# Optimization experiments

Hardware: AMD Instinct MI355X
Metric: run time of the kernel (lower is better)

The kernel has to match this reference:

```python
import jax, jax.numpy as jnp
import numpy as np

N_NODES = 50000
N_EDGES = 800000
NUM_RELATIONS = 8   # 2 * n_speakers**2 with n_speakers = 2
NUM_BASES = 30
G_DIM, H1_DIM, H2_DIM = 128, 128, 128


def setup_inputs() -> dict:
    key = jax.random.key(0)
    ks = jax.random.split(key, 10)
    inp = {
        "node_features": jax.random.normal(ks[0], (N_NODES, G_DIM), jnp.float32),
        "edge_index": jax.random.randint(ks[1], (2, N_EDGES), 0, N_NODES, dtype=jnp.int64),
        "edge_type": jax.random.randint(ks[2], (N_EDGES,), 0, NUM_RELATIONS, dtype=jnp.int64),
        "edge_norm": jax.random.uniform(ks[3], (N_EDGES,), jnp.float32),
        # RGCNConv params (basis decomposition)
        "basis": jax.random.normal(ks[4], (NUM_BASES, G_DIM, H1_DIM), jnp.float32) * 0.05,
        "comp": jax.random.normal(ks[5], (NUM_RELATIONS, NUM_BASES), jnp.float32) * 0.1,
        "root": jax.random.normal(ks[6], (G_DIM, H1_DIM), jnp.float32) * 0.05,
        "bias1": jnp.zeros((H1_DIM,), jnp.float32),
        # GraphConv params: lin_rel (with bias) applied to aggregated neighbors, lin_root (no bias)
        "w_rel": jax.random.normal(ks[7], (H1_DIM, H2_DIM), jnp.float32) * 0.05,
        "b_rel": jnp.zeros((H2_DIM,), jnp.float32),
        "w_root": jax.random.normal(ks[8], (H1_DIM, H2_DIM), jnp.float32) * 0.05,
    }
    return inp


def reference(node_features, edge_index, edge_type, edge_norm,
              basis, comp, root, bias1, w_rel, b_rel, w_root):
    src, dst = edge_index[0], edge_index[1]  # source_to_target flow (PyG default)

    # ---- Layer 1: RGCNConv with basis decomposition ----
    # W[r] = sum_b comp[r,b] * basis[b]  -> [R, g, h1]
    W = jnp.einsum('rb,bio->rio', comp, basis)
    # Project every node under every relation once (N*R*h1), then gather per edge.
    # Mathematically identical to per-edge x_j @ W[edge_type] but avoids an [E, g, h1] tensor.
    x_proj = jnp.einsum('ni,rio->nro', node_features, W)  # [N, R, h1]
    msg = x_proj[src, edge_type] * edge_norm[:, None]     # [E, h1]
    agg = jax.ops.segment_sum(msg, dst, num_segments=N_NODES)  # scatter-add to targets
    h = agg + node_features @ root + bias1                # [N, h1]

    # ---- Layer 2: GraphConv (aggr='add', no edge_weight) ----
    agg2 = jax.ops.segment_sum(h[src], dst, num_segments=N_NODES)  # [N, h1]
    out = agg2 @ w_rel + b_rel + h @ w_root               # [N, h2]
    return out
```

## Files before the change

### kernel.cpp

```cpp
#include <hip/hip_runtime.h>
#include <hip/hip_bf16.h>
#include <stdint.h>

#define N_NODES 50000
#define N_EDGES 800000
#define NREL    8
#define NBASES  30
#define DIM     128
#define NSLOT   9
#define NCAT    (NSLOT*DIM)
#define SCAN_NB ((N_NODES + 255) / 256)

typedef __attribute__((ext_vector_type(8))) short short8;
typedef __attribute__((ext_vector_type(4))) float floatx4;
typedef __hip_bfloat16  bf16;
typedef __hip_bfloat162 bf16x2;

__device__ inline ushort f2bu(float f) { bf16 b = __float2bfloat16(f); return *(ushort*)&b; }
__device__ inline float  bu2f(ushort u) { union { unsigned i; float f; } c; c.i = ((unsigned)u) << 16; return c.f; }

__global__ void prep_weights(const float* __restrict__ basis, const float* __restrict__ comp,
                             const float* __restrict__ root, const float* __restrict__ w_rel,
                             const float* __restrict__ w_root,
                             bf16* __restrict__ WcatT, bf16* __restrict__ wrelT, bf16* __restrict__ wrootT) {
    int idx = blockIdx.x * blockDim.x + threadIdx.x;
    const int n_cat = NCAT * DIM;
    const int n_sq  = DIM * DIM;
    if (idx < n_cat) {
        int k = idx & 127, n = idx >> 7;
        int r = n >> 7, o = n & 127;
        float v;
        if (r < NREL) {
            v = 0.f;
            for (int b = 0; b < NBASES; ++b)
                v += comp[r * NBASES + b] * basis[(b * DIM + k) * DIM + o];
        } else {
            v = root[k * DIM + o];
        }
        WcatT[n * DIM + k] = __float2bfloat16(v);
    } else if (idx < n_cat + n_sq) {
        int t = idx - n_cat; int k = t & 127, o = t >> 7;
        wrelT[o * DIM + k] = __float2bfloat16(w_rel[k * DIM + o]);
    } else if (idx < n_cat + 2 * n_sq) {
        int t = idx - n_cat - n_sq; int k = t & 127, o = t >> 7;
        wrootT[o * DIM + k] = __float2bfloat16(w_root[k * DIM + o]);
    }
}

__global__ void conv_x(const float4* __restrict__ x4, ushort4* __restrict__ xb4, int n4) {
    int i = blockIdx.x * blockDim.x + threadIdx.x;
    if (i < n4) {
        float4 f = x4[i];
        ushort4 o;
        o.x = f2bu(f.x); o.y = f2bu(f.y); o.z = f2bu(f.z); o.w = f2bu(f.w);
        xb4[i] = o;
    }
}

__global__ void hist_kernel(const int* __restrict__ ei, int* __restrict__ deg) {
    int e = blockIdx.x * blockDim.x + threadIdx.x;
    if (e < N_EDGES) atomicAdd(&deg[ei[N_EDGES + e]], 1);
}

__global__ void scan_blocks(const int* __restrict__ deg, int* __restrict__ segoff,
                            int* __restrict__ bsum, int n) {
    __shared__ int buf[256];
    int tid = threadIdx.x;
    int i = blockIdx.x * 256 + tid;
    int v = (i < n) ? deg[i] : 0;
    buf[tid] = v;
    __syncthreads();
#pragma unroll
    for (int o = 1; o < 256; o <<= 1) {
        int t = (tid >= o) ? buf[tid - o] : 0;
        __syncthreads();
        buf[tid] += t;
        __syncthreads();
    }
    if (i < n) segoff[i + 1] = buf[tid];
    if (tid == 255) bsum[blockIdx.x] = buf[255];
}

__global__ void scan_sums(int* __restrict__ bsum, int nb) {
    int lane = threadIdx.x;
    int base = 0;
    for (int start = 0; start < nb; start += 64) {
        int i = start + lane;
        int v = (i < nb) ? bsum[i] : 0;
        int incl = v;
#pragma unroll
        for (int o = 1; o < 64; o <<= 1) {
            int t = __shfl_up(incl, o, 64);
            if (lane >= o) incl += t;
        }
        if (i < nb) bsum[i] = base + incl - v;
        base += __shfl(incl, 63, 64);
    }
}

__global__ void scan_add(int* __restrict__ segoff, const int* __restrict__ bsum, int n) {
    int i = blockIdx.x * 256 + threadIdx.x;
    if (i < n) segoff[i + 1] += bsum[blockIdx.x];
    if (i == 0) segoff[0] = 0;
}

__global__ void scatter_kernel(const int* __restrict__ ei, const int* __restrict__ et,
                               const float* __restrict__ en, const int* __restrict__ segoff,
                               int* __restrict__ cur, uint2* __restrict__ rec) {
    int e = blockIdx.x * blockDim.x + threadIdx.x;
    if (e < N_EDGES) {
        int d = ei[N_EDGES + e];
        int p = segoff[d] + atomicAdd(&cur[d], 1);
        rec[p] = make_uint2((unsigned)ei[e] | ((unsigned)et[e] << 16), __float_as_uint(en[e]));
    }
}

__global__ __launch_bounds__(256) void gemm1_kernel(const bf16* __restrict__ A, const bf16* __restrict__ BT,
                                                    bf16* __restrict__ C, int M) {
    __shared__ ushort As[64][136];
    __shared__ ushort Bs[64][136];
    const ushort* Au = (const ushort*)A;
    const ushort* Bu = (const ushort*)BT;
    ushort* Cu = (ushort*)C;
    int tm = blockIdx.x * 64;
    int wave = threadIdx.x >> 6, lane = threadIdx.x & 63;
    int q = lane >> 4, mr = lane & 15;

#pragma unroll
    for (int u = 0; u < 4; ++u) {
        int cc = threadIdx.x + u * 256;
        int row = cc >> 4, seg = cc & 15;
        int gr = tm + row;
        short8 av = {0, 0, 0, 0, 0, 0, 0, 0};
        if (gr < M) av = *(const short8*)(Au + (size_t)gr * 128 + seg * 8);
        *(short8*)(&As[row][seg * 8]) = av;
    }

    floatx4 zero = {0.f, 0.f, 0.f, 0.f};
    for (int t = 0; t < 18; ++t) {
        if (t) __syncthreads();
#pragma unroll
        for (int u = 0; u < 4; ++u) {
            int cc = threadIdx.x + u * 256;
            int row = cc >> 4, seg = cc & 15;
            short8 bv = *(const short8*)(Bu + (size_t)(t * 64 + row) * 128 + seg * 8);
            *(short8*)(&Bs[row][seg * 8]) = bv;
        }
        __syncthreads();
        floatx4 acc[4] = {zero, zero, zero, zero};
#pragma unroll
        for (int kt = 0; kt < 4; ++kt) {
            short8 a = *(const short8*)(&As[wave * 16 + mr][q * 8 + kt * 32]);
#pragma unroll
            for (int nt = 0; nt < 4; ++nt) {
                short8 b = *(const short8*)(&Bs[nt * 16 + mr][q * 8 + kt * 32]);
                acc[nt] = __builtin_amdgcn_mfma_f32_16x16x32_bf16(a, b, acc[nt], 0, 0, 0);
            }
        }
#pragma unroll
        for (int nt = 0; nt < 4; ++nt)
#pragma unroll
            for (int r4 = 0; r4 < 4; ++r4) {
                int row = tm + wave * 16 + q * 4 + r4;
                if (row < M) Cu[(size_t)row * NCAT + t * 64 + nt * 16 + mr] = f2bu(acc[nt][r4]);
            }
    }
}

__global__ void seg1_kernel(const uint2* __restrict__ rec, const int* __restrict__ segoff,
                            const ushort* __restrict__ proj, const float* __restrict__ bias1,
                            ushort* __restrict__ h) {
    int quad = threadIdx.x >> 4;
    int node = blockIdx.x * 16 + quad;
    if (node >= N_NODES) return;
    int lane = threadIdx.x & 15;
    int s = segoff[node], e = segoff[node + 1];
    float acc[8] = {0.f, 0.f, 0.f, 0.f, 0.f, 0.f, 0.f, 0.f};
    for (int chunk = s; chunk < e; chunk += 4) {
        int m = e - chunk; if (m > 4) m = 4;
        uint2 rr[4]; short8 vv[4];
#pragma unroll
        for (int j = 0; j < 4; ++j) if (j < m) rr[j] = rec[chunk + j];
#pragma unroll
        for (int j = 0; j < 4; ++j) if (j < m) {
            unsigned src = rr[j].x & 0xFFFFu;
            unsigned typ = rr[j].x >> 16;
            vv[j] = *(const short8*)(proj + ((size_t)src * NSLOT + typ) * 128 + lane * 8);
        }
#pragma unroll
        for (int j = 0; j < 4; ++j) if (j < m) {
            float norm = __uint_as_float(rr[j].y);
#pragma unroll
            for (int f = 0; f < 8; ++f) acc[f] += norm * bu2f((ushort)vv[j][f]);
        }
    }
    short8 base = *(const short8*)(proj + ((size_t)node * NSLOT + 8) * 128 + lane * 8);
    short8 o;
#pragma unroll
    for (int f = 0; f < 8; ++f)
        o[f] = (short)f2bu(acc[f] + bu2f((ushort)base[f]) + bias1[lane * 8 + f]);
    *(short8*)(h + (size_t)node * 128 + lane * 8) = o;
}

__global__ void seg2_kernel(const uint2* __restrict__ rec, const int* __restrict__ segoff,
                            const ushort* __restrict__ h, ushort* __restrict__ out2) {
    int quad = threadIdx.x >> 4;
    int node = blockIdx.x * 16 + quad;
    if (node >= N_NODES) return;
    int lane = threadIdx.x & 15;
    int s = segoff[node], e = segoff[node + 1];
    float acc[8] = {0.f, 0.f, 0.f, 0.f, 0.f, 0.f, 0.f, 0.f};
    for (int chunk = s; chunk < e; chunk += 4) {
        int m = e - chunk; if (m > 4) m = 4;
        uint2 rr[4]; short8 vv[4];
#pragma unroll
        for (int j = 0; j < 4; ++j) if (j < m) rr[j] = rec[chunk + j];
#pragma unroll
        for (int j = 0; j < 4; ++j) if (j < m)
            vv[j] = *(const short8*)(h + (size_t)(rr[j].x & 0xFFFFu) * 128 + lane * 8);
#pragma unroll
        for (int j = 0; j < 4; ++j) if (j < m)
#pragma unroll
            for (int f = 0; f < 8; ++f) acc[f] += bu2f((ushort)vv[j][f]);
    }
    short8 o;
#pragma unroll
    for (int f = 0; f < 8; ++f) o[f] = (short)f2bu(acc[f]);
    *(short8*)(out2 + (size_t)node * 128 + lane * 8) = o;
}

__global__ __launch_bounds__(256) void gemm2_kernel(const bf16* __restrict__ A1, const bf16* __restrict__ B1T,
                                                    const bf16* __restrict__ A2, const bf16* __restrict__ B2T,
                                                    const float* __restrict__ brel, float* __restrict__ out, int M) {
    __shared__ ushort As[64][136];
    __shared__ ushort Bs[64][136];
    int tm = blockIdx.x * 64, tn = blockIdx.y * 64;
    int wave = threadIdx.x >> 6, lane = threadIdx.x & 63;
    int q = lane >> 4, mr = lane & 15;
    floatx4 zero = {0.f, 0.f, 0.f, 0.f};
    floatx4 acc[4] = {zero, zero, zero, zero};

    for (int phase = 0; phase < 2; ++phase) {
        const ushort* Au = (const ushort*)(phase ? A2 : A1);
        const ushort* Bu = (const ushort*)(phase ? B2T : B1T);
        if (phase) __syncthreads();
        for (int c = threadIdx.x; c < 64 * 16; c += 256) {
            int row = c >> 4, seg = c & 15;
            int gr = tm + row;
            short8 av = {0, 0, 0, 0, 0, 0, 0, 0};
            if (gr < M) av = *(const short8*)(Au + (size_t)gr * 128 + seg * 8);
            *(short8*)(&As[row][seg * 8]) = av;
            short8 bv = *(const short8*)(Bu + (size_t)(tn + row) * 128 + seg * 8);
            *(short8*)(&Bs[row][seg * 8]) = bv;
        }
        __syncthreads();
#pragma unroll
        for (int kt = 0; kt < 4; ++kt) {
            short8 a = *(const short8*)(&As[wave * 16 + mr][q * 8 + kt * 32]);
#pragma unroll
            for (int nt = 0; nt < 4; ++nt) {
                short8 b = *(const short8*)(&Bs[nt * 16 + mr][q * 8 + kt * 32]);
                acc[nt] = __builtin_amdgcn_mfma_f32_16x16x32_bf16(a, b, acc[nt], 0, 0, 0);
            }
        }
    }
    __syncthreads();
    float* Csf = (float*)&As[0][0];
#pragma unroll
    for (int nt = 0; nt < 4; ++nt)
#pragma unroll
        for (int r4 = 0; r4 < 4; ++r4) {
            int row = wave * 16 + q * 4 + r4;
            int col = nt * 16 + mr;
            Csf[row * 68 + col] = acc[nt][r4] + brel[tn + col];
        }
    __syncthreads();
#pragma unroll
    for (int u = 0; u < 4; ++u) {
        int cc = threadIdx.x + u * 256;
        int row = cc >> 4, seg = cc & 15;
        int gr = tm + row;
        if (gr < M) {
            float4 v = *(const float4*)(&Csf[row * 68 + seg * 4]);
            *(float4*)(out + (size_t)gr * 128 + tn + seg * 4) = v;
        }
    }
}

extern "C" void kernel_launch(void* const* d_in, const int* in_sizes, int n_in,
                              void* d_out, int out_size, void* d_ws, size_t ws_size,
                              hipStream_t stream) {
    const float* x      = (const float*)d_in[0];
    const int*   ei     = (const int*)d_in[1];
    const int*   et     = (const int*)d_in[2];
    const float* en     = (const float*)d_in[3];
    const float* basis  = (const float*)d_in[4];
    const float* comp   = (const float*)d_in[5];
    const float* root   = (const float*)d_in[6];
    const float* bias1  = (const float*)d_in[7];
    const float* w_rel  = (const float*)d_in[8];
    const float* b_rel  = (const float*)d_in[9];
    const float* w_root = (const float*)d_in[10];
    float* out = (float*)d_out;

    char* ws = (char*)d_ws;
    size_t off = 0;
    auto alloc = [&](size_t bytes) { size_t o = off; off += (bytes + 255) & ~(size_t)255; return o; };

    size_t o_deg    = alloc((size_t)N_NODES * 4);
    size_t o_cur    = alloc((size_t)N_NODES * 4);
    size_t o_segoff = alloc((size_t)(N_NODES + 1) * 4);
    size_t o_bsum   = alloc((size_t)SCAN_NB * 4);
    size_t o_rec    = alloc((size_t)N_EDGES * 8);
    size_t o_wcat   = alloc((size_t)NCAT * DIM * 2);
    size_t o_wrel   = alloc((size_t)DIM * DIM * 2);
    size_t o_wroot  = alloc((size_t)DIM * DIM * 2);
    size_t o_xb     = alloc((size_t)N_NODES * DIM * 2);
    size_t o_proj   = alloc((size_t)N_NODES * NCAT * 2);
    size_t o_hb     = alloc((size_t)N_NODES * DIM * 2);
    size_t o_agg2   = alloc((size_t)N_NODES * DIM * 2);

    int*   deg    = (int*)(ws + o_deg);
    int*   cur    = (int*)(ws + o_cur);
    int*   segoff = (int*)(ws + o_segoff);
    int*   bsum   = (int*)(ws + o_bsum);
    uint2* rec    = (uint2*)(ws + o_rec);
    bf16*  wcat   = (bf16*)(ws + o_wcat);
    bf16*  wrelT  = (bf16*)(ws + o_wrel);
    bf16*  wrootT = (bf16*)(ws + o_wroot);
    bf16*  xb     = (bf16*)(ws + o_xb);
    bf16*  proj   = (bf16*)(ws + o_proj);
    bf16*  hb     = (bf16*)(ws + o_hb);
    bf16*  agg2   = (bf16*)(ws + o_agg2);

    hipMemsetAsync(ws + o_deg, 0, o_segoff - o_deg, stream);

    {
        int total = NCAT * DIM + 2 * DIM * DIM;
        prep_weights<<<(total + 255) / 256, 256, 0, stream>>>(basis, comp, root, w_rel, w_root,
                                                              wcat, wrelT, wrootT);
    }
    {
        int n4 = N_NODES * DIM / 4;
        conv_x<<<(n4 + 255) / 256, 256, 0, stream>>>((const float4*)x, (ushort4*)xb, n4);
    }
    hist_kernel<<<(N_EDGES + 255) / 256, 256, 0, stream>>>(ei, deg);
    scan_blocks<<<SCAN_NB, 256, 0, stream>>>(deg, segoff, bsum, N_NODES);
    scan_sums<<<1, 64, 0, stream>>>(bsum, SCAN_NB);
    scan_add<<<SCAN_NB, 256, 0, stream>>>(segoff, bsum, N_NODES);
    scatter_kernel<<<(N_EDGES + 255) / 256, 256, 0, stream>>>(ei, et, en, segoff, cur, rec);

    gemm1_kernel<<<(N_NODES + 63) / 64, 256, 0, stream>>>(xb, wcat, proj, N_NODES);
    seg1_kernel<<<(N_NODES + 15) / 16, 256, 0, stream>>>(rec, segoff, (const ushort*)proj, bias1, (ushort*)hb);
    seg2_kernel<<<(N_NODES + 15) / 16, 256, 0, stream>>>(rec, segoff, (const ushort*)hb, (ushort*)agg2);
    {
        dim3 grid((N_NODES + 63) / 64, DIM / 64);
        gemm2_kernel<<<grid, 256, 0, stream>>>(agg2, wrelT, hb, wrootT, b_rel, out, N_NODES);
    }
}
```

Measured before the change: 336.1 us.

## Replace global atomic edge scatter with two-pass bucketed counting sort

The per-edge scatter that used one global atomic per edge on a per-node counter becomes a two-pass placement. The first pass buckets edges into coarse chunks of 256 destination nodes using shared-memory histograms and one global atomic per block and bucket. The second pass sorts each bucket into per-node segments using shared-memory atomics. This is meant to cut global atomic contention and scattered writes, at the cost of an extra 6.4MB temp buffer, an extra kernel launch, and packing the local destination into the record's high bits.

After: 328.6 us. 1.02x faster.

```diff
diff --git a/kernel.cpp b/kernel.cpp
--- a/kernel.cpp
+++ b/kernel.cpp
@@ -10,6 +10,9 @@
 #define NSLOT   9
 #define NCAT    (NSLOT*DIM)
 #define SCAN_NB ((N_NODES + 255) / 256)
+#define NB_C    196
+#define EPB_PLACE 2048
+#define NBLK_PLACE ((N_EDGES + EPB_PLACE - 1) / EPB_PLACE)
 
 typedef __attribute__((ext_vector_type(8))) short short8;
 typedef __attribute__((ext_vector_type(4))) float floatx4;
@@ -104,14 +107,54 @@
     if (i == 0) segoff[0] = 0;
 }
 
-__global__ void scatter_kernel(const int* __restrict__ ei, const int* __restrict__ et,
-                               const float* __restrict__ en, const int* __restrict__ segoff,
-                               int* __restrict__ cur, uint2* __restrict__ rec) {
-    int e = blockIdx.x * blockDim.x + threadIdx.x;
-    if (e < N_EDGES) {
-        int d = ei[N_EDGES + e];
-        int p = segoff[d] + atomicAdd(&cur[d], 1);
-        rec[p] = make_uint2((unsigned)ei[e] | ((unsigned)et[e] << 16), __float_as_uint(en[e]));
+__global__ __launch_bounds__(256) void place_kernel(const int* __restrict__ ei, const int* __restrict__ et,
+                                                    const float* __restrict__ en, const int* __restrict__ segoff,
+                                                    int* __restrict__ bcur, uint2* __restrict__ tmp) {
+    __shared__ int lhist[NB_C];
+    __shared__ int lbase[NB_C];
+    __shared__ int lrank[NB_C];
+    int tid = threadIdx.x;
+    for (int i = tid; i < NB_C; i += 256) { lhist[i] = 0; lrank[i] = 0; }
+    __syncthreads();
+    int e0 = blockIdx.x * EPB_PLACE;
+#pragma unroll
+    for (int i = 0; i < EPB_PLACE / 256; ++i) {
+        int e = e0 + i * 256 + tid;
+        if (e < N_EDGES) atomicAdd(&lhist[ei[N_EDGES + e] >> 8], 1);
+    }
+    __syncthreads();
+    for (int c = tid; c < NB_C; c += 256)
+        if (lhist[c] > 0) lbase[c] = atomicAdd(&bcur[c], lhist[c]);
+    __syncthreads();
+#pragma unroll
+    for (int i = 0; i < EPB_PLACE / 256; ++i) {
+        int e = e0 + i * 256 + tid;
+        if (e < N_EDGES) {
+            int d = ei[N_EDGES + e];
+            int c = d >> 8;
+            int r = atomicAdd(&lrank[c], 1);
+            int p = segoff[c << 8] + lbase[c] + r;
+            tmp[p] = make_uint2((unsigned)ei[e] | ((unsigned)et[e] << 16) | ((unsigned)(d & 255) << 19),
+                                __float_as_uint(en[e]));
+        }
+    }
+}
+
+__global__ __launch_bounds__(256) void sortb_kernel(const uint2* __restrict__ tmp, const int* __restrict__ segoff,
+                                                    uint2* __restrict__ rec) {
+    __shared__ int cur[256];
+    int c = blockIdx.x;
+    int tid = threadIdx.x;
+    cur[tid] = 0;
+    __syncthreads();
+    int base = segoff[c << 8];
+    int nlimit = (c + 1) << 8; if (nlimit > N_NODES) nlimit = N_NODES;
+    int end = segoff[nlimit];
+    for (int i = base + tid; i < end; i += 256) {
+        uint2 r = tmp[i];
+        int dl = (r.x >> 19) & 255;
+        int p = segoff[(c << 8) + dl] + atomicAdd(&cur[dl], 1);
+        rec[p] = make_uint2(r.x & 0x7FFFFu, r.y);
     }
 }
 
@@ -308,10 +351,11 @@
     auto alloc = [&](size_t bytes) { size_t o = off; off += (bytes + 255) & ~(size_t)255; return o; };
 
     size_t o_deg    = alloc((size_t)N_NODES * 4);
-    size_t o_cur    = alloc((size_t)N_NODES * 4);
+    size_t o_bcur   = alloc((size_t)NB_C * 4);
     size_t o_segoff = alloc((size_t)(N_NODES + 1) * 4);
     size_t o_bsum   = alloc((size_t)SCAN_NB * 4);
     size_t o_rec    = alloc((size_t)N_EDGES * 8);
+    size_t o_tmp    = alloc((size_t)N_EDGES * 8);
     size_t o_wcat   = alloc((size_t)NCAT * DIM * 2);
     size_t o_wrel   = alloc((size_t)DIM * DIM * 2);
     size_t o_wroot  = alloc((size_t)DIM * DIM * 2);
@@ -321,10 +365,11 @@
     size_t o_agg2   = alloc((size_t)N_NODES * DIM * 2);
 
     int*   deg    = (int*)(ws + o_deg);
-    int*   cur    = (int*)(ws + o_cur);
+    int*   bcur   = (int*)(ws + o_bcur);
     int*   segoff = (int*)(ws + o_segoff);
     int*   bsum   = (int*)(ws + o_bsum);
     uint2* rec    = (uint2*)(ws + o_rec);
+    uint2* tmp    = (uint2*)(ws + o_tmp);
     bf16*  wcat   = (bf16*)(ws + o_wcat);
     bf16*  wrelT  = (bf16*)(ws + o_wrel);
     bf16*  wrootT = (bf16*)(ws + o_wroot);
@@ -348,7 +393,8 @@
     scan_blocks<<<SCAN_NB, 256, 0, stream>>>(deg, segoff, bsum, N_NODES);
     scan_sums<<<1, 64, 0, stream>>>(bsum, SCAN_NB);
     scan_add<<<SCAN_NB, 256, 0, stream>>>(segoff, bsum, N_NODES);
-    scatter_kernel<<<(N_EDGES + 255) / 256, 256, 0, stream>>>(ei, et, en, segoff, cur, rec);
+    place_kernel<<<NBLK_PLACE, 256, 0, stream>>>(ei, et, en, segoff, bcur, tmp);
+    sortb_kernel<<<NB_C, 256, 0, stream>>>(tmp, segoff, rec);
 
     gemm1_kernel<<<(N_NODES + 63) / 64, 256, 0, stream>>>(xb, wcat, proj, N_NODES);
     seg1_kernel<<<(N_NODES + 15) / 16, 256, 0, stream>>>(rec, segoff, (const ushort*)proj, bias1, (ushort*)hb);
```
